# Performance work log

Hardware: AMD Instinct MI355X
Metric: run time of the kernel (lower is better)

The kernel has to match this reference:

```python
import jax, jax.numpy as jnp
import numpy as np

IN_DIM = 128
OUT_DIM = 128
H = 8
HD = OUT_DIM // H  # 16
EPS = 1e-5
NEG = -1e30


def setup_inputs() -> dict:
    key = jax.random.key(0)
    ks = jax.random.split(key, 10)
    B, N = 8, 1024
    h = jax.random.normal(ks[0], (B, N, IN_DIM), dtype=jnp.float32)
    adj_mask = jax.random.randint(ks[1], (B, N, N), 0, 2, dtype=jnp.int32)
    s = 1.0 / np.sqrt(IN_DIM)
    W = jax.random.normal(ks[2], (H, IN_DIM, HD), dtype=jnp.float32) * s
    a = jax.random.normal(ks[3], (H, 2 * HD), dtype=jnp.float32) * (1.0 / np.sqrt(2 * HD))
    ln1_g = jnp.ones((OUT_DIM,), jnp.float32)
    ln1_b = jnp.zeros((OUT_DIM,), jnp.float32)
    w1 = jax.random.normal(ks[4], (OUT_DIM, 2 * OUT_DIM), dtype=jnp.float32) * (1.0 / np.sqrt(OUT_DIM))
    b1 = jnp.zeros((2 * OUT_DIM,), jnp.float32)
    w2 = jax.random.normal(ks[5], (2 * OUT_DIM, OUT_DIM), dtype=jnp.float32) * (1.0 / np.sqrt(2 * OUT_DIM))
    b2 = jnp.zeros((OUT_DIM,), jnp.float32)
    ln2_g = jnp.ones((OUT_DIM,), jnp.float32)
    ln2_b = jnp.zeros((OUT_DIM,), jnp.float32)
    return dict(h=h, adj_mask=adj_mask, W=W, a=a, ln1_g=ln1_g, ln1_b=ln1_b,
                w1=w1, b1=b1, w2=w2, b2=b2, ln2_g=ln2_g, ln2_b=ln2_b)


def _layernorm(x, g, b):
    mu = jnp.mean(x, axis=-1, keepdims=True)
    var = jnp.mean(jnp.square(x - mu), axis=-1, keepdims=True)
    return (x - mu) * jax.lax.rsqrt(var + EPS) * g + b


def reference(h, adj_mask, W, a, ln1_g, ln1_b, w1, b1, w2, b2, ln2_g, ln2_b):
    B, N, _ = h.shape
    # Per-head projection: (B,H,N,HD)
    Wh = jnp.einsum('bni,hid->bhnd', h, W)
    # a.[Wh_i, Wh_j] = a_src.Wh_i + a_dst.Wh_j (decompose concat-score)
    a_src, a_dst = a[:, :HD], a[:, HD:]
    s_i = jnp.einsum('bhnd,hd->bhn', Wh, a_src)  # source term
    s_j = jnp.einsum('bhnd,hd->bhn', Wh, a_dst)  # target term
    e = s_i[:, :, :, None] + s_j[:, :, None, :]  # (B,H,N,N)
    e = jnp.where(e >= 0, e, 0.2 * e)            # LeakyReLU(0.2)
    mask = (adj_mask != 0)[:, None, :, :]        # (B,1,N,N)
    e = jnp.where(mask, e, NEG)
    alpha = jax.nn.softmax(e, axis=-1)
    # rows with no neighbors -> NaN in torch softmax -> zeroed; replicate
    row_valid = jnp.any(mask, axis=-1, keepdims=True)  # (B,1,N,1)
    alpha = jnp.where(row_valid, alpha, 0.0)
    # dropout in eval mode = identity
    h_heads = jnp.einsum('bhnm,bhmd->bhnd', alpha, Wh)
    h_cat = h_heads.transpose(0, 2, 1, 3).reshape(B, N, H * HD)
    # residual (in_dim == out_dim here)
    h_cat = _layernorm(h_cat + h, ln1_g, ln1_b)
    ffn = jnp.maximum(h_cat @ w1 + b1, 0.0) @ w2 + b2
    return _layernorm(h_cat + ffn, ln2_g, ln2_b)
```

## Files before the change

### kernel.cpp

```cpp
#include <hip/hip_runtime.h>
#include <hip/hip_bf16.h>

#define IN_DIM 128
#define OUT_DIM 128
#define NHEAD 8
#define HD 16
#define BB 8
#define NN 1024
#define LOG2E 1.44269504f

typedef unsigned long long u64;
typedef float f32x4 __attribute__((ext_vector_type(4)));
typedef short bf16x8 __attribute__((ext_vector_type(8)));

__global__ __launch_bounds__(256) void k_prep(
    const float* __restrict__ hin, const float* __restrict__ W,
    const float* __restrict__ a, const int* __restrict__ adj,
    u64* __restrict__ bits, unsigned short* __restrict__ whT,
    float* __restrict__ si_g, float* __restrict__ sj_g,
    const float* __restrict__ w1, const float* __restrict__ w2,
    unsigned short* __restrict__ w1T, unsigned short* __restrict__ w2T)
{
    __shared__ float smem[32 * 132];
    int blk = blockIdx.x;
    int t = threadIdx.x;

    if (blk < 256) {
        int b = blk >> 5, ntile = blk & 31;
        const float* hrow = hin + ((size_t)b * NN + ntile * 32) * IN_DIM;
#pragma unroll
        for (int it = 0; it < 4; ++it) {
            int g = t + 256 * it;
            int row = g >> 5, c4 = g & 31;
            float4 v = ((const float4*)hrow)[g];
            *(float4*)&smem[row * 132 + c4 * 4] = v;
        }
        __syncthreads();

        int d4 = t & 3;
        int hq = (t >> 2) & 7;
        int ngrp = t >> 5;
        float acc[4][4];
#pragma unroll
        for (int q = 0; q < 4; ++q)
#pragma unroll
            for (int dd = 0; dd < 4; ++dd) acc[q][dd] = 0.f;

        for (int i4 = 0; i4 < 32; ++i4) {
            float4 wf[4];
#pragma unroll
            for (int k = 0; k < 4; ++k)
                wf[k] = *(const float4*)&W[((size_t)hq * 128 + i4 * 4 + k) * 16 + d4 * 4];
            float4 hv[4];
#pragma unroll
            for (int q = 0; q < 4; ++q)
                hv[q] = *(const float4*)&smem[(ngrp * 4 + q) * 132 + i4 * 4];
#pragma unroll
            for (int q = 0; q < 4; ++q) {
                acc[q][0] += hv[q].x * wf[0].x + hv[q].y * wf[1].x + hv[q].z * wf[2].x + hv[q].w * wf[3].x;
                acc[q][1] += hv[q].x * wf[0].y + hv[q].y * wf[1].y + hv[q].z * wf[2].y + hv[q].w * wf[3].y;
                acc[q][2] += hv[q].x * wf[0].z + hv[q].y * wf[1].z + hv[q].z * wf[2].z + hv[q].w * wf[3].z;
                acc[q][3] += hv[q].x * wf[0].w + hv[q].y * wf[1].w + hv[q].z * wf[2].w + hv[q].w * wf[3].w;
            }
        }

        int bh = b * NHEAD + hq;
        int rowbase = ntile * 32 + ngrp * 4;

        float asrc[4], adst[4];
#pragma unroll
        for (int dd = 0; dd < 4; ++dd) {
            asrc[dd] = a[hq * 32 + d4 * 4 + dd];
            adst[dd] = a[hq * 32 + 16 + d4 * 4 + dd];
        }
#pragma unroll
        for (int q = 0; q < 4; ++q) {
            float psi = acc[q][0] * asrc[0] + acc[q][1] * asrc[1] + acc[q][2] * asrc[2] + acc[q][3] * asrc[3];
            float psj = acc[q][0] * adst[0] + acc[q][1] * adst[1] + acc[q][2] * adst[2] + acc[q][3] * adst[3];
            psi += __shfl_xor(psi, 1); psi += __shfl_xor(psi, 2);
            psj += __shfl_xor(psj, 1); psj += __shfl_xor(psj, 2);
            if (d4 == 0) {
                si_g[(size_t)bh * NN + rowbase + q] = psi * LOG2E;
                sj_g[(size_t)bh * NN + rowbase + q] = psj * LOG2E;
            }
        }

#pragma unroll
        for (int dd = 0; dd < 4; ++dd) {
            unsigned u0, u1;
            asm("v_cvt_pk_bf16_f32 %0, %1, %2" : "=v"(u0) : "v"(acc[0][dd]), "v"(acc[1][dd]));
            asm("v_cvt_pk_bf16_f32 %0, %1, %2" : "=v"(u1) : "v"(acc[2][dd]), "v"(acc[3][dd]));
            uint2 pk = make_uint2(u0, u1);
            *(uint2*)&whT[((size_t)bh * 16 + d4 * 4 + dd) * 1024 + rowbase] = pk;
        }
    } else if (blk < 2304) {
        int lane = t & 63;
        int wid = (blk - 256) * 4 + (t >> 6);
        for (int w = wid; w < BB * NN * 16; w += 2048 * 4) {
            int v = adj[(size_t)w * 64 + lane];
            u64 m = __ballot(v != 0);
            if (lane == 0) bits[w] = m;
        }
    } else {
        int bb = blk - 2304;
        const float* src; unsigned short* dst; int R, C;
        if (bb < 32) { src = w1; dst = w1T; R = 128; C = 256; }
        else         { src = w2; dst = w2T; R = 256; C = 128; bb -= 32; }
        int tpr = C >> 5;
        int tr = bb / tpr, tc = bb - tr * tpr;
        int r0 = tr << 5, c0 = tc << 5;
        int lr = t >> 5, lc = t & 31;
#pragma unroll
        for (int p = 0; p < 4; ++p)
            smem[(lr + p * 8) * 33 + lc] = src[(size_t)(r0 + lr + p * 8) * C + c0 + lc];
        __syncthreads();
#pragma unroll
        for (int p = 0; p < 4; ++p) {
            __hip_bfloat16 bv = __float2bfloat16(smem[lc * 33 + lr + p * 8]);
            dst[(size_t)(c0 + lr + p * 8) * R + r0 + lc] = *(unsigned short*)&bv;
        }
    }
}

__global__ __launch_bounds__(512, 3) void k_attn(
    const unsigned short* __restrict__ whT,
    const unsigned* __restrict__ bits32,
    const float* __restrict__ si_g, const float* __restrict__ sj_g,
    float* __restrict__ hh)
{
    __shared__ __align__(16) unsigned short whT_s[16 * 1032];
    __shared__ __align__(16) float sj_s[NN];
    int t = threadIdx.x;
    int blk = blockIdx.x;
    int part = blk & 7;
    int bh = blk >> 3;
    int hq = bh & 7, b = bh >> 3;
    int blkrow = part * 128;

    {
        const uint4* src = (const uint4*)(whT + (size_t)bh * 16 * 1024);
#pragma unroll
        for (int it = 0; it < 4; ++it) {
            int g = t + 512 * it;
            int d = g >> 7, c8 = g & 127;
            uint4 v = src[g];
            *(uint4*)&whT_s[d * 1032 + ((c8 ^ (d & 3)) * 8)] = v;
        }
        if (t < 256) *(float4*)&sj_s[t * 4] = ((const float4*)(sj_g + (size_t)bh * NN))[t];
    }
    __syncthreads();

    int wv = t >> 6, lane = t & 63;
    int lo16 = lane & 15, g = lane >> 4;
    int row = blkrow + wv * 16 + lo16;
    float si_r = si_g[(size_t)bh * NN + row];
    const unsigned* mrow = bits32 + ((size_t)b * NN + row) * 32;

    f32x4 acc = {0.f, 0.f, 0.f, 0.f};
    float lsum = 0.f;
    unsigned m = mrow[0];
#pragma unroll 4
    for (int kt = 0; kt < 32; ++kt) {
        unsigned m_next = (kt < 31) ? mrow[kt + 1] : 0u;
        bf16x8 bfrag = *(const bf16x8*)&whT_s[lo16 * 1032 + (((kt * 4 + g) ^ (lo16 & 3)) * 8)];
        float4 sa = *(const float4*)&sj_s[kt * 32 + g * 8];
        float4 sb = *(const float4*)&sj_s[kt * 32 + g * 8 + 4];
        unsigned mm = m >> (g * 8);
        float sj[8] = {sa.x, sa.y, sa.z, sa.w, sb.x, sb.y, sb.z, sb.w};
        float p[8];
#pragma unroll
        for (int e = 0; e < 8; ++e) {
            float v = si_r + sj[e];
            float lv = __builtin_fmaf(0.4f, __builtin_fabsf(v), 0.6f * v);
            lv = ((mm >> e) & 1) ? lv : -150.f;
            float pe;
            asm("v_exp_f32 %0, %1" : "=v"(pe) : "v"(lv));
            lsum += pe;
            p[e] = pe;
        }
        union { bf16x8 v; unsigned u[4]; } af;
#pragma unroll
        for (int q = 0; q < 4; ++q)
            asm("v_cvt_pk_bf16_f32 %0, %1, %2" : "=v"(af.u[q]) : "v"(p[2 * q]), "v"(p[2 * q + 1]));
        acc = __builtin_amdgcn_mfma_f32_16x16x32_bf16(af.v, bfrag, acc, 0, 0, 0);
        m = m_next;
    }

    lsum += __shfl_xor(lsum, 16);
    lsum += __shfl_xor(lsum, 32);

    float* obase = hh + ((size_t)b * NN + blkrow + wv * 16) * OUT_DIM + hq * HD + lo16;
#pragma unroll
    for (int q = 0; q < 4; ++q) {
        float ls = __shfl(lsum, 4 * g + q);
        float r = (ls > 0.f) ? 1.0f / ls : 0.f;
        obase[(size_t)(4 * g + q) * OUT_DIM] = acc[q] * r;
    }
}

__global__ __launch_bounds__(512, 1) void k_ffn(const float* __restrict__ hhs,
                                                const float* __restrict__ hin,
                                                const float* __restrict__ g1,
                                                const float* __restrict__ bt1,
                                                const unsigned short* __restrict__ w1T,
                                                const float* __restrict__ bb1,
                                                const unsigned short* __restrict__ w2T,
                                                const float* __restrict__ bb2,
                                                const float* __restrict__ g2,
                                                const float* __restrict__ bt2,
                                                float* __restrict__ out) {
    __shared__ float xc_f[32][128];
    __shared__ float y_f[32][132];
    __shared__ __align__(16) unsigned short xc_bf[32 * 128];
    __shared__ __align__(16) unsigned short hid_bf[32 * 256];

    int t = threadIdx.x;
    int R0 = blockIdx.x * 32;
    int wv = t >> 6, lane = t & 63;
    int lo = lane & 15, g = lane >> 4;

    bf16x8 b1f[2][4];
#pragma unroll
    for (int jt = 0; jt < 2; ++jt) {
        int n = (wv * 2 + jt) * 16 + lo;
#pragma unroll
        for (int kt = 0; kt < 4; ++kt)
            b1f[jt][kt] = *(const bf16x8*)&w1T[(size_t)n * 128 + kt * 32 + g * 8];
    }
    bf16x8 b2f[8];
    {
        int n = wv * 16 + lo;
#pragma unroll
        for (int kt = 0; kt < 8; ++kt)
            b2f[kt] = *(const bf16x8*)&w2T[(size_t)n * 256 + kt * 32 + g * 8];
    }
    float b1v[2];
    b1v[0] = bb1[(wv * 2 + 0) * 16 + lo];
    b1v[1] = bb1[(wv * 2 + 1) * 16 + lo];
    float b2v = bb2[wv * 16 + lo];

    {
        int r = t >> 4, c = t & 15;
        size_t row = (size_t)(R0 + r) * 128;
        float4 ha = *(const float4*)&hhs[row + c * 8];
        float4 hb = *(const float4*)&hhs[row + c * 8 + 4];
        float4 ia = *(const float4*)&hin[row + c * 8];
        float4 ib = *(const float4*)&hin[row + c * 8 + 4];
        float x[8] = {ha.x + ia.x, ha.y + ia.y, ha.z + ia.z, ha.w + ia.w,
                      hb.x + ib.x, hb.y + ib.y, hb.z + ib.z, hb.w + ib.w};
        float s = 0.f, s2 = 0.f;
#pragma unroll
        for (int j = 0; j < 8; ++j) { s += x[j]; s2 += x[j] * x[j]; }
#pragma unroll
        for (int off = 8; off > 0; off >>= 1) {
            s += __shfl_xor(s, off);
            s2 += __shfl_xor(s2, off);
        }
        float mu = s * (1.f / 128.f);
        float var = s2 * (1.f / 128.f) - mu * mu;
        float rs = rsqrtf(var + 1e-5f);
        float4 ga = *(const float4*)&g1[c * 8], gb = *(const float4*)&g1[c * 8 + 4];
        float4 ba = *(const float4*)&bt1[c * 8], bb = *(const float4*)&bt1[c * 8 + 4];
        float gg[8] = {ga.x, ga.y, ga.z, ga.w, gb.x, gb.y, gb.z, gb.w};
        float bbv[8] = {ba.x, ba.y, ba.z, ba.w, bb.x, bb.y, bb.z, bb.w};
        float xo[8];
#pragma unroll
        for (int j = 0; j < 8; ++j) xo[j] = (x[j] - mu) * rs * gg[j] + bbv[j];
        *(float4*)&xc_f[r][c * 8]     = make_float4(xo[0], xo[1], xo[2], xo[3]);
        *(float4*)&xc_f[r][c * 8 + 4] = make_float4(xo[4], xo[5], xo[6], xo[7]);
        union { uint4 v; unsigned u[4]; } pk;
#pragma unroll
        for (int q = 0; q < 4; ++q)
            asm("v_cvt_pk_bf16_f32 %0, %1, %2" : "=v"(pk.u[q]) : "v"(xo[2 * q]), "v"(xo[2 * q + 1]));
        int byte = (r * 256 + c * 16) ^ ((r & 7) << 4);
        *(uint4*)((char*)xc_bf + byte) = pk.v;
    }
    __syncthreads();

    {
        bf16x8 af[2][4];
#pragma unroll
        for (int mt = 0; mt < 2; ++mt) {
            int m = mt * 16 + lo;
#pragma unroll
            for (int kt = 0; kt < 4; ++kt) {
                int byte = (m * 256 + kt * 64 + g * 16) ^ ((m & 7) << 4);
                af[mt][kt] = *(const bf16x8*)((const char*)xc_bf + byte);
            }
        }
#pragma unroll
        for (int mt = 0; mt < 2; ++mt)
#pragma unroll
            for (int jt = 0; jt < 2; ++jt) {
                f32x4 acc = {0.f, 0.f, 0.f, 0.f};
#pragma unroll
                for (int kt = 0; kt < 4; ++kt)
                    acc = __builtin_amdgcn_mfma_f32_16x16x32_bf16(af[mt][kt], b1f[jt][kt], acc, 0, 0, 0);
                int n = (wv * 2 + jt) * 16 + lo;
#pragma unroll
                for (int q = 0; q < 4; ++q) {
                    float hv = fmaxf(acc[q] + b1v[jt], 0.f);
                    int m = mt * 16 + 4 * g + q;
                    int byte = (m * 512 + n * 2) ^ ((m & 7) << 4);
                    __hip_bfloat16 bv = __float2bfloat16(hv);
                    *(unsigned short*)((char*)hid_bf + byte) = *(unsigned short*)&bv;
                }
            }
    }
    __syncthreads();

    {
        f32x4 acc2[2] = {{0.f, 0.f, 0.f, 0.f}, {0.f, 0.f, 0.f, 0.f}};
#pragma unroll
        for (int mt = 0; mt < 2; ++mt) {
            int m = mt * 16 + lo;
#pragma unroll
            for (int kt = 0; kt < 8; ++kt) {
                int byte = (m * 512 + kt * 64 + g * 16) ^ ((m & 7) << 4);
                bf16x8 a = *(const bf16x8*)((const char*)hid_bf + byte);
                acc2[mt] = __builtin_amdgcn_mfma_f32_16x16x32_bf16(a, b2f[kt], acc2[mt], 0, 0, 0);
            }
        }
        int n = wv * 16 + lo;
#pragma unroll
        for (int mt = 0; mt < 2; ++mt)
#pragma unroll
            for (int q = 0; q < 4; ++q)
                y_f[mt * 16 + 4 * g + q][n] = acc2[mt][q] + b2v;
    }
    __syncthreads();

    {
        int r = t >> 4, c = t & 15;
        float xv[8];
        float s = 0.f, s2 = 0.f;
#pragma unroll
        for (int j = 0; j < 8; ++j) {
            float v = xc_f[r][c * 8 + j] + y_f[r][c * 8 + j];
            xv[j] = v; s += v; s2 += v * v;
        }
#pragma unroll
        for (int off = 8; off > 0; off >>= 1) {
            s += __shfl_xor(s, off);
            s2 += __shfl_xor(s2, off);
        }
        float mu = s * (1.f / 128.f);
        float var = s2 * (1.f / 128.f) - mu * mu;
        float rs = rsqrtf(var + 1e-5f);
        float4 ga = *(const float4*)&g2[c * 8], gb = *(const float4*)&g2[c * 8 + 4];
        float4 ba = *(const float4*)&bt2[c * 8], bb = *(const float4*)&bt2[c * 8 + 4];
        float o[8] = {(xv[0] - mu) * rs * ga.x + ba.x, (xv[1] - mu) * rs * ga.y + ba.y,
                      (xv[2] - mu) * rs * ga.z + ba.z, (xv[3] - mu) * rs * ga.w + ba.w,
                      (xv[4] - mu) * rs * gb.x + bb.x, (xv[5] - mu) * rs * gb.y + bb.y,
                      (xv[6] - mu) * rs * gb.z + bb.z, (xv[7] - mu) * rs * gb.w + bb.w};
        size_t row = (size_t)(R0 + r) * 128;
        *(float4*)&out[row + c * 8]     = make_float4(o[0], o[1], o[2], o[3]);
        *(float4*)&out[row + c * 8 + 4] = make_float4(o[4], o[5], o[6], o[7]);
    }
}

extern "C" void kernel_launch(void* const* d_in, const int* in_sizes, int n_in,
                              void* d_out, int out_size, void* d_ws, size_t ws_size,
                              hipStream_t stream) {
    const float* hin  = (const float*)d_in[0];
    const int*   adj  = (const int*)d_in[1];
    const float* W    = (const float*)d_in[2];
    const float* a    = (const float*)d_in[3];
    const float* ln1g = (const float*)d_in[4];
    const float* ln1b = (const float*)d_in[5];
    const float* w1   = (const float*)d_in[6];
    const float* b1   = (const float*)d_in[7];
    const float* w2   = (const float*)d_in[8];
    const float* b2   = (const float*)d_in[9];
    const float* ln2g = (const float*)d_in[10];
    const float* ln2b = (const float*)d_in[11];
    float* out = (float*)d_out;

    u64* bits           = (u64*)d_ws;
    unsigned short* whT = (unsigned short*)((char*)d_ws + (1u << 20));
    float* si_g         = (float*)((char*)d_ws + (3u << 20));
    float* sj_g         = (float*)((char*)d_ws + (3u << 20) + (256u << 10));
    float* hh           = (float*)((char*)d_ws + (3u << 20) + (512u << 10));
    unsigned short* w1T = (unsigned short*)((char*)d_ws + (7u << 20) + (512u << 10));
    unsigned short* w2T = (unsigned short*)((char*)d_ws + (7u << 20) + (512u << 10) + 65536);

    k_prep<<<2368, 256, 0, stream>>>(hin, W, a, adj, bits, whT, si_g, sj_g,
                                     w1, w2, w1T, w2T);
    k_attn<<<BB * NHEAD * 8, 512, 0, stream>>>(whT, (const unsigned*)bits, si_g, sj_g, hh);
    k_ffn<<<BB * NN / 32, 512, 0, stream>>>(hh, hin, ln1g, ln1b, w1T, b1, w2T, b2, ln2g, ln2b, out);
}
```

Measured before the change: 62.90 us.

## Transpose adjacency bitmask to column-major and drop LDS swizzle in attention

The prep kernel now stores the adjacency bitmask as 32-bit words transposed so that consecutive rows of the same word index are adjacent. In the attention kernel, lanes reading different rows then make coalesced loads instead of 128-byte-strided ones. The XOR swizzle on the shared-memory copy of the transposed Wh is removed, relying on the 1032-element row padding to avoid bank conflicts. The softmax inner loop is rewritten to process pairs and read sj from shared memory as scalars rather than float4, which may raise LDS instruction count.

```diff
diff --git a/kernel.cpp b/kernel.cpp
--- a/kernel.cpp
+++ b/kernel.cpp
@@ -16,7 +16,7 @@
 __global__ __launch_bounds__(256) void k_prep(
     const float* __restrict__ hin, const float* __restrict__ W,
     const float* __restrict__ a, const int* __restrict__ adj,
-    u64* __restrict__ bits, unsigned short* __restrict__ whT,
+    unsigned* __restrict__ bits_t, unsigned short* __restrict__ whT,
     float* __restrict__ si_g, float* __restrict__ sj_g,
     const float* __restrict__ w1, const float* __restrict__ w2,
     unsigned short* __restrict__ w1T, unsigned short* __restrict__ w2T)
@@ -99,7 +99,12 @@
         for (int w = wid; w < BB * NN * 16; w += 2048 * 4) {
             int v = adj[(size_t)w * 64 + lane];
             u64 m = __ballot(v != 0);
-            if (lane == 0) bits[w] = m;
+            if (lane == 0) {
+                int b = w >> 14, i = (w >> 4) & 1023, k = w & 15;
+                unsigned* dst = bits_t + ((size_t)b * 32 + k * 2) * 1024 + i;
+                dst[0] = (unsigned)m;
+                dst[1024] = (unsigned)(m >> 32);
+            }
         }
     } else {
         int bb = blk - 2304;
@@ -124,7 +129,7 @@
 
 __global__ __launch_bounds__(512, 3) void k_attn(
     const unsigned short* __restrict__ whT,
-    const unsigned* __restrict__ bits32,
+    const unsigned* __restrict__ bits_t,
     const float* __restrict__ si_g, const float* __restrict__ sj_g,
     float* __restrict__ hh)
 {
@@ -144,7 +149,7 @@
             int g = t + 512 * it;
             int d = g >> 7, c8 = g & 127;
             uint4 v = src[g];
-            *(uint4*)&whT_s[d * 1032 + ((c8 ^ (d & 3)) * 8)] = v;
+            *(uint4*)&whT_s[d * 1032 + c8 * 8] = v;
         }
         if (t < 256) *(float4*)&sj_s[t * 4] = ((const float4*)(sj_g + (size_t)bh * NN))[t];
     }
@@ -154,34 +159,32 @@
     int lo16 = lane & 15, g = lane >> 4;
     int row = blkrow + wv * 16 + lo16;
     float si_r = si_g[(size_t)bh * NN + row];
-    const unsigned* mrow = bits32 + ((size_t)b * NN + row) * 32;
+    const unsigned* mcol = bits_t + (size_t)b * 32 * 1024 + row;
 
     f32x4 acc = {0.f, 0.f, 0.f, 0.f};
     float lsum = 0.f;
-    unsigned m = mrow[0];
+    unsigned m = mcol[0];
 #pragma unroll 4
     for (int kt = 0; kt < 32; ++kt) {
-        unsigned m_next = (kt < 31) ? mrow[kt + 1] : 0u;
-        bf16x8 bfrag = *(const bf16x8*)&whT_s[lo16 * 1032 + (((kt * 4 + g) ^ (lo16 & 3)) * 8)];
-        float4 sa = *(const float4*)&sj_s[kt * 32 + g * 8];
-        float4 sb = *(const float4*)&sj_s[kt * 32 + g * 8 + 4];
+        unsigned m_next = (kt < 31) ? mcol[(size_t)(kt + 1) * 1024] : 0u;
+        bf16x8 bfrag = *(const bf16x8*)&whT_s[lo16 * 1032 + kt * 32 + g * 8];
         unsigned mm = m >> (g * 8);
-        float sj[8] = {sa.x, sa.y, sa.z, sa.w, sb.x, sb.y, sb.z, sb.w};
-        float p[8];
-#pragma unroll
-        for (int e = 0; e < 8; ++e) {
-            float v = si_r + sj[e];
-            float lv = __builtin_fmaf(0.4f, __builtin_fabsf(v), 0.6f * v);
-            lv = ((mm >> e) & 1) ? lv : -150.f;
-            float pe;
-            asm("v_exp_f32 %0, %1" : "=v"(pe) : "v"(lv));
-            lsum += pe;
-            p[e] = pe;
-        }
+        const float* sjp = &sj_s[kt * 32 + g * 8];
         union { bf16x8 v; unsigned u[4]; } af;
 #pragma unroll
-        for (int q = 0; q < 4; ++q)
-            asm("v_cvt_pk_bf16_f32 %0, %1, %2" : "=v"(af.u[q]) : "v"(p[2 * q]), "v"(p[2 * q + 1]));
+        for (int e2 = 0; e2 < 4; ++e2) {
+            float v0 = si_r + sjp[2 * e2];
+            float v1 = si_r + sjp[2 * e2 + 1];
+            float lv0 = __builtin_fmaf(0.4f, __builtin_fabsf(v0), 0.6f * v0);
+            float lv1 = __builtin_fmaf(0.4f, __builtin_fabsf(v1), 0.6f * v1);
+            lv0 = ((mm >> (2 * e2)) & 1) ? lv0 : -150.f;
+            lv1 = ((mm >> (2 * e2 + 1)) & 1) ? lv1 : -150.f;
+            float p0, p1;
+            asm("v_exp_f32 %0, %1" : "=v"(p0) : "v"(lv0));
+            asm("v_exp_f32 %0, %1" : "=v"(p1) : "v"(lv1));
+            lsum += p0 + p1;
+            asm("v_cvt_pk_bf16_f32 %0, %1, %2" : "=v"(af.u[e2]) : "v"(p0), "v"(p1));
+        }
         acc = __builtin_amdgcn_mfma_f32_16x16x32_bf16(af.v, bfrag, acc, 0, 0, 0);
         m = m_next;
     }
@@ -376,7 +379,7 @@
     const float* ln2b = (const float*)d_in[11];
     float* out = (float*)d_out;
 
-    u64* bits           = (u64*)d_ws;
+    unsigned* bits_t    = (unsigned*)d_ws;
     unsigned short* whT = (unsigned short*)((char*)d_ws + (1u << 20));
     float* si_g         = (float*)((char*)d_ws + (3u << 20));
     float* sj_g         = (float*)((char*)d_ws + (3u << 20) + (256u << 10));
@@ -384,8 +387,8 @@
     unsigned short* w1T = (unsigned short*)((char*)d_ws + (7u << 20) + (512u << 10));
     unsigned short* w2T = (unsigned short*)((char*)d_ws + (7u << 20) + (512u << 10) + 65536);
 
-    k_prep<<<2368, 256, 0, stream>>>(hin, W, a, adj, bits, whT, si_g, sj_g,
+    k_prep<<<2368, 256, 0, stream>>>(hin, W, a, adj, bits_t, whT, si_g, sj_g,
                                      w1, w2, w1T, w2T);
-    k_attn<<<BB * NHEAD * 8, 512, 0, stream>>>(whT, (const unsigned*)bits, si_g, sj_g, hh);
+    k_attn<<<BB * NHEAD * 8, 512, 0, stream>>>(whT, bits_t, si_g, sj_g, hh);
     k_ffn<<<BB * NN / 32, 512, 0, stream>>>(hh, hin, ln1g, ln1b, w1T, b1, w2T, b2, ln2g, ln2b, out);
 }
```

Measured after the change: 62.60 us. About the same (-0.5%).
